# Kernel optimization log

Hardware: AMD Instinct MI355X
Metric: run time of the kernel (lower is better)

Reference implementation:

```python
import jax, jax.numpy as jnp
import numpy as np

EMBED = 1024
HEADS = 16
HEAD_DIM = EMBED // HEADS


def setup_inputs() -> dict:
    key = jax.random.key(0)
    ks = jax.random.split(key, 7)
    N, L = 2, 2048
    values = jax.random.normal(ks[0], (N, L, EMBED), dtype=jnp.float32)
    keys = jax.random.normal(ks[1], (N, L, EMBED), dtype=jnp.float32)
    queries = jax.random.normal(ks[2], (N, L, EMBED), dtype=jnp.float32)
    mask = jax.random.randint(ks[3], (N, 1, L, L), 0, 2, dtype=jnp.int32)
    s = 1.0 / np.sqrt(HEAD_DIM)
    Wv = jax.random.normal(ks[4], (HEAD_DIM, HEAD_DIM), dtype=jnp.float32) * s
    Wk = jax.random.normal(ks[5], (HEAD_DIM, HEAD_DIM), dtype=jnp.float32) * s
    Wq = jax.random.normal(ks[6], (HEAD_DIM, HEAD_DIM), dtype=jnp.float32) * s
    return {"values": values, "keys": keys, "queries": queries, "mask": mask,
            "Wv": Wv, "Wk": Wk, "Wq": Wq}


def reference(values, keys, queries, mask, Wv, Wk, Wq):
    N, Lq = queries.shape[0], queries.shape[1]
    Lk = keys.shape[1]
    # reshape to [N, L, H, D]; nn.Linear(x) = x @ W.T (shared across heads)
    v = values.reshape(N, Lk, HEADS, HEAD_DIM) @ Wv.T
    k = keys.reshape(N, Lk, HEADS, HEAD_DIM) @ Wk.T
    q = queries.reshape(N, Lq, HEADS, HEAD_DIM) @ Wq.T
    # scores scaled by sqrt(embed_size) as in the original module
    e = jnp.einsum("nqhd,nkhd->nhqk", q, k) / jnp.sqrt(jnp.float32(EMBED))
    e = jnp.where(mask == 0, jnp.float32(-1e20), e)
    attn = jax.nn.softmax(e, axis=-1)
    out = jnp.einsum("nhqk,nkhd->nqhd", attn, v)
    return out.reshape(N, Lq, HEADS * HEAD_DIM)
```

## Files before the change

### kernel.cpp

```cpp
#include <hip/hip_runtime.h>
#include <hip/hip_bf16.h>

#define LSEQ 2048
#define NB   2
#define NH   16
#define HD   64
#define NKT  32
#define QSCALE 0.04508687049285173f

typedef __attribute__((ext_vector_type(8))) __bf16 bf16x8;
typedef __attribute__((ext_vector_type(4))) __bf16 bf16x4;
typedef __attribute__((ext_vector_type(2))) __bf16 bf16x2;
typedef __attribute__((ext_vector_type(4))) float  f32x4;

__global__ __launch_bounds__(256)
void pack_mask_kernel(const int* __restrict__ mask,
                      unsigned long long* __restrict__ mbits) {
  size_t gw = ((size_t)blockIdx.x * 256 + threadIdx.x) >> 6;
  int lane = threadIdx.x & 63;
  int v = mask[gw * 64 + lane];
  unsigned long long b = __ballot(v != 0);
  if (lane == 0) mbits[gw] = b;
}

__global__ __launch_bounds__(256)
void proj_kernel(const float* __restrict__ xv, const float* __restrict__ Wv_,
                 const float* __restrict__ xk, const float* __restrict__ Wk_,
                 const float* __restrict__ xq, const float* __restrict__ Wq_,
                 __bf16* __restrict__ outv, __bf16* __restrict__ outk,
                 __bf16* __restrict__ outq) {
  __shared__ __bf16 S[16384];
  __bf16* Xh = S;
  __bf16* Xl = S + 4096;
  __bf16* Wh = S + 8192;
  __bf16* Wl = S + 12288;

  const float* x; const float* W; __bf16* out;
  if (blockIdx.z == 0)      { x = xv; W = Wv_; out = outv; }
  else if (blockIdx.z == 1) { x = xk; W = Wk_; out = outk; }
  else                      { x = xq; W = Wq_; out = outq; }
  const float osc = (blockIdx.z == 2) ? QSCALE : 1.0f;

  const int tid = threadIdx.x;
  const int bx = blockIdx.x;
  const int h  = blockIdx.y;
  const int n  = bx >> 5;
  const int l0 = (bx & 31) << 6;

  const int r  = tid >> 2;
  const int c0 = (tid & 3) << 4;
  const float* xrow = x + ((size_t)(n * LSEQ + l0) + r) * 1024 + h * 64 + c0;
  const float* wrow = W + r * 64 + c0;

#pragma unroll
  for (int hf = 0; hf < 2; ++hf) {
    int kc = c0 + hf * 8;
    int off = r * 64 + (kc ^ ((r & 7) << 3));
    float4 a = *(const float4*)(xrow + hf * 8);
    float4 b = *(const float4*)(xrow + hf * 8 + 4);
    float va[8] = {a.x, a.y, a.z, a.w, b.x, b.y, b.z, b.w};
    bf16x8 hi, lo;
#pragma unroll
    for (int j = 0; j < 8; ++j) {
      __bf16 h_ = (__bf16)va[j];
      hi[j] = h_;
      lo[j] = (__bf16)(va[j] - (float)h_);
    }
    *(bf16x8*)(Xh + off) = hi;
    *(bf16x8*)(Xl + off) = lo;

    float4 c = *(const float4*)(wrow + hf * 8);
    float4 d = *(const float4*)(wrow + hf * 8 + 4);
    float vw[8] = {c.x, c.y, c.z, c.w, d.x, d.y, d.z, d.w};
    bf16x8 whv, wlv;
#pragma unroll
    for (int j = 0; j < 8; ++j) {
      __bf16 h_ = (__bf16)vw[j];
      whv[j] = h_;
      wlv[j] = (__bf16)(vw[j] - (float)h_);
    }
    *(bf16x8*)(Wh + off) = whv;
    *(bf16x8*)(Wl + off) = wlv;
  }
  __syncthreads();

  const int wv   = tid >> 6;
  const int lane = tid & 63;
  const int l15  = lane & 15;
  const int lhi  = lane >> 4;

  bf16x8 xhf[2], xlf[2];
  const int arow = wv * 16 + l15;
#pragma unroll
  for (int ko = 0; ko < 2; ++ko) {
    int aoff = arow * 64 + ((ko * 32 + lhi * 8) ^ ((arow & 7) << 3));
    xhf[ko] = *(const bf16x8*)(Xh + aoff);
    xlf[ko] = *(const bf16x8*)(Xl + aoff);
  }

  f32x4 acc[4] = {};
#pragma unroll
  for (int cg = 0; cg < 4; ++cg) {
    int d = cg * 16 + l15;
#pragma unroll
    for (int ko = 0; ko < 2; ++ko) {
      int boff = d * 64 + ((ko * 32 + lhi * 8) ^ ((d & 7) << 3));
      bf16x8 whf = *(const bf16x8*)(Wh + boff);
      bf16x8 wlf = *(const bf16x8*)(Wl + boff);
      acc[cg] = __builtin_amdgcn_mfma_f32_16x16x32_bf16(xhf[ko], whf, acc[cg], 0, 0, 0);
      acc[cg] = __builtin_amdgcn_mfma_f32_16x16x32_bf16(xhf[ko], wlf, acc[cg], 0, 0, 0);
      acc[cg] = __builtin_amdgcn_mfma_f32_16x16x32_bf16(xlf[ko], whf, acc[cg], 0, 0, 0);
    }
  }
  __syncthreads();

  __bf16* tb = S;
#pragma unroll
  for (int cg = 0; cg < 4; ++cg)
#pragma unroll
    for (int rr = 0; rr < 4; ++rr)
      tb[(wv * 16 + lhi * 4 + rr) * 72 + cg * 16 + l15] = (__bf16)(acc[cg][rr] * osc);
  __syncthreads();

  const int tok = tid >> 2;
  const int d0  = (tid & 3) * 16;
  bf16x8 o0 = *(const bf16x8*)(tb + tok * 72 + d0);
  bf16x8 o1 = *(const bf16x8*)(tb + tok * 72 + d0 + 8);
  size_t ob = (size_t)(n * NH + h) * LSEQ + l0;
  *(bf16x8*)(out + (ob + tok) * HD + d0)     = o0;
  *(bf16x8*)(out + (ob + tok) * HD + d0 + 8) = o1;
}

__global__ __launch_bounds__(256)
void attn_kernel(const __bf16* __restrict__ Qb, const __bf16* __restrict__ Kb,
                 const __bf16* __restrict__ Vb,
                 const unsigned long long* __restrict__ mbits,
                 float* __restrict__ out) {
  __shared__ __bf16 Ks[2][64 * 64];
  __shared__ __bf16 Vts[2][64 * 64];

  const int tid  = threadIdx.x;
  const int wid  = tid >> 6;
  const int lane = tid & 63;
  const int l15  = lane & 15;
  const int lhi  = lane >> 4;

  const int lin = blockIdx.y * 16 + blockIdx.x;
  const int xcd = lin & 7;
  const int idx = lin >> 3;
  const int nh  = xcd + ((idx >> 4) << 3);
  const int qt  = idx & 15;
  const int n   = nh >> 4;
  const int h   = nh & 15;
  const int q0  = qt << 7;

  const __bf16* Qg = Qb + ((size_t)nh * LSEQ + q0) * HD;
  const __bf16* Kg = Kb + (size_t)nh * LSEQ * HD;
  const __bf16* Vg = Vb + (size_t)nh * LSEQ * HD;

  bf16x8 qf[2][2];
#pragma unroll
  for (int mi = 0; mi < 2; ++mi)
#pragma unroll
    for (int ks = 0; ks < 2; ++ks)
      qf[mi][ks] = *(const bf16x8*)(Qg + (size_t)(wid * 32 + mi * 16 + l15) * HD
                                       + ks * 32 + lhi * 8);

  f32x4 o[2][4] = {};
  f32x4 o_ls[2] = {};
  const unsigned long long* mrow0 =
      mbits + ((size_t)n * LSEQ + q0 + wid * 32 + l15) * NKT;
  const unsigned long long* mrow1 = mrow0 + (size_t)16 * NKT;

  bf16x8 onesf;
#pragma unroll
  for (int j = 0; j < 8; ++j) onesf[j] = (__bf16)1.0f;

  const int vkg  = lane & 15;
  const int vdgw = (wid << 2) + lhi;
  const int vslotbase = ((vkg & 8) << 2) + ((vkg & 3) << 3) + (((vkg >> 2) & 1) << 2);
  bf16x4 vv[4];

#define STAGE_K(kt_, buf_)                                                         \
  _Pragma("unroll")                                                                \
  for (int it = 0; it < 2; ++it) {                                                 \
    int chb = wid * 64 + it * 256;                                                 \
    int ch = chb + lane;                                                           \
    int skey = ch >> 3, sdc = ch & 7;                                              \
    const __bf16* src = Kg + (size_t)(kt_) * 4096 + skey * 64 + ((sdc ^ (skey & 7)) << 3); \
    __builtin_amdgcn_global_load_lds(                                              \
        (const __attribute__((address_space(1))) void*)src,                        \
        (__attribute__((address_space(3))) void*)(&Ks[buf_][chb * 8]), 16, 0, 0);  \
  }
#define LOAD_V(kt_)                                                                \
  _Pragma("unroll")                                                                \
  for (int m_ = 0; m_ < 4; ++m_)                                                   \
    vv[m_] = *(const bf16x4*)(Vg + (size_t)(kt_) * 4096 + (vkg * 4 + m_) * HD + vdgw * 4);
#define WRITE_V(buf_)                                                              \
  _Pragma("unroll")                                                                \
  for (int i = 0; i < 4; ++i) {                                                    \
    int d = vdgw * 4 + i;                                                          \
    int swz = (d & 7) ^ ((d >> 3) & 7);                                            \
    bf16x4 pr; pr[0] = vv[0][i]; pr[1] = vv[1][i]; pr[2] = vv[2][i]; pr[3] = vv[3][i]; \
    *(bf16x4*)(&Vts[buf_][d * 64 + (vslotbase ^ (swz << 3))]) = pr;                \
  }

  STAGE_K(0, 0);
  LOAD_V(0);
  WRITE_V(0);
  unsigned long long w0 = mrow0[0];
  unsigned long long w1 = mrow1[0];
  __syncthreads();

  for (int kt = 0; kt < NKT; ++kt) {
    const int cur = kt & 1;
    const int nxt = cur ^ 1;
    const bool pf = (kt + 1 < NKT);
    unsigned long long nw0 = 0, nw1 = 0;
    if (pf) {
      STAGE_K(kt + 1, nxt);
      LOAD_V(kt + 1);
      nw0 = mrow0[kt + 1];
      nw1 = mrow1[kt + 1];
    }

    f32x4 s[2][4] = {};
#pragma unroll
    for (int ks = 0; ks < 2; ++ks)
#pragma unroll
      for (int t = 0; t < 4; ++t) {
        int key = t * 16 + l15;
        bf16x8 kf = *(const bf16x8*)(
            &Ks[cur][key * 64 + ((ks * 32 + lhi * 8) ^ ((key & 7) << 3))]);
        s[0][t] = __builtin_amdgcn_mfma_f32_16x16x32_bf16(kf, qf[0][ks], s[0][t], 0, 0, 0);
        s[1][t] = __builtin_amdgcn_mfma_f32_16x16x32_bf16(kf, qf[1][ks], s[1][t], 0, 0, 0);
      }

    bf16x8 pa[2][2];
#pragma unroll
    for (int mi = 0; mi < 2; ++mi) {
      unsigned long long w = mi ? w1 : w0;
      unsigned long long wsh = w >> (lhi * 4);
      unsigned shl = (unsigned)wsh;
      unsigned shh = (unsigned)(wsh >> 32);
#pragma unroll
      for (int t = 0; t < 4; ++t) {
        unsigned sh = (t < 2) ? shl : shh;
#pragma unroll
        for (int r = 0; r < 4; ++r) {
          float p = __builtin_amdgcn_exp2f(s[mi][t][r]);
          p = ((sh >> ((t & 1) * 16 + r)) & 1u) ? p : 0.f;
          pa[mi][t >> 1][(t & 1) * 4 + r] = (__bf16)p;
        }
      }
    }

    if (pf) { WRITE_V(nxt); }

#pragma unroll
    for (int ks = 0; ks < 2; ++ks) {
#pragma unroll
      for (int t = 0; t < 4; ++t) {
        int d = t * 16 + l15;
        int swz = (d & 7) ^ ((d >> 3) & 7);
        bf16x8 vf = *(const bf16x8*)(
            &Vts[cur][d * 64 + ((ks * 32 + lhi * 8) ^ (swz << 3))]);
        o[0][t] = __builtin_amdgcn_mfma_f32_16x16x32_bf16(pa[0][ks], vf, o[0][t], 0, 0, 0);
        o[1][t] = __builtin_amdgcn_mfma_f32_16x16x32_bf16(pa[1][ks], vf, o[1][t], 0, 0, 0);
      }
      o_ls[0] = __builtin_amdgcn_mfma_f32_16x16x32_bf16(pa[0][ks], onesf, o_ls[0], 0, 0, 0);
      o_ls[1] = __builtin_amdgcn_mfma_f32_16x16x32_bf16(pa[1][ks], onesf, o_ls[1], 0, 0, 0);
    }

    w0 = nw0;
    w1 = nw1;
    __syncthreads();
  }

#pragma unroll
  for (int mi = 0; mi < 2; ++mi) {
    float inv[4];
#pragma unroll
    for (int r = 0; r < 4; ++r)
      inv[r] = 1.f / o_ls[mi][r];
#pragma unroll
    for (int r = 0; r < 4; ++r) {
      size_t ob = ((size_t)n * LSEQ + q0 + wid * 32 + mi * 16 + lhi * 4 + r) * 1024
                + h * 64 + l15;
#pragma unroll
      for (int t = 0; t < 4; ++t)
        out[ob + t * 16] = o[mi][t][r] * inv[r];
    }
  }
#undef STAGE_K
#undef LOAD_V
#undef WRITE_V
}

extern "C" void kernel_launch(void* const* d_in, const int* in_sizes, int n_in,
                              void* d_out, int out_size, void* d_ws, size_t ws_size,
                              hipStream_t stream) {
  const float* xv   = (const float*)d_in[0];
  const float* xk   = (const float*)d_in[1];
  const float* xq   = (const float*)d_in[2];
  const int*   mask = (const int*)d_in[3];
  const float* Wv   = (const float*)d_in[4];
  const float* Wk   = (const float*)d_in[5];
  const float* Wq   = (const float*)d_in[6];
  float* out = (float*)d_out;

  const size_t elems = (size_t)NB * NH * LSEQ * HD;
  __bf16* Qw = (__bf16*)d_ws;
  __bf16* Kw = Qw + elems;
  __bf16* Vw = Kw + elems;
  unsigned long long* mb = (unsigned long long*)(Vw + elems);

  pack_mask_kernel<<<dim3(NB * LSEQ * NKT / 4), 256, 0, stream>>>(mask, mb);
  proj_kernel<<<dim3(64, NH, 3), 256, 0, stream>>>(xv, Wv, xk, Wk, xq, Wq,
                                                   Vw, Kw, Qw);
  attn_kernel<<<dim3(16, 32), 256, 0, stream>>>(Qw, Kw, Vw, mb, out);
}
```

Baseline: 104.5 us.

## Split key tile across two wave groups with LDS reduction of partial outputs

Doubles the attention block to 512 threads. Two groups of four waves each take half of every 64-key tile for the same 128 queries. One group stages K and the other loads and transposes V, which splits the producer work between them. The partial O accumulators and row sums are then combined through LDS at the end. The aim is more waves in flight and shorter per-wave dependency chains, at the cost of an extra reduction pass and higher register and occupancy pressure.

```diff
diff --git a/kernel.cpp b/kernel.cpp
--- a/kernel.cpp
+++ b/kernel.cpp
@@ -131,16 +131,18 @@
   *(bf16x8*)(out + (ob + tok) * HD + d0 + 8) = o1;
 }
 
-__global__ __launch_bounds__(256)
+__global__ __launch_bounds__(512, 4)
 void attn_kernel(const __bf16* __restrict__ Qb, const __bf16* __restrict__ Kb,
                  const __bf16* __restrict__ Vb,
                  const unsigned long long* __restrict__ mbits,
                  float* __restrict__ out) {
-  __shared__ __bf16 Ks[2][64 * 64];
-  __shared__ __bf16 Vts[2][64 * 64];
+  __shared__ __bf16 KV[16384];
+  __shared__ float  Ls[128];
 
   const int tid  = threadIdx.x;
   const int wid  = tid >> 6;
+  const int hw   = wid >> 2;
+  const int wq   = wid & 3;
   const int lane = tid & 63;
   const int l15  = lane & 15;
   const int lhi  = lane >> 4;
@@ -163,13 +165,13 @@
   for (int mi = 0; mi < 2; ++mi)
 #pragma unroll
     for (int ks = 0; ks < 2; ++ks)
-      qf[mi][ks] = *(const bf16x8*)(Qg + (size_t)(wid * 32 + mi * 16 + l15) * HD
+      qf[mi][ks] = *(const bf16x8*)(Qg + (size_t)(wq * 32 + mi * 16 + l15) * HD
                                        + ks * 32 + lhi * 8);
 
   f32x4 o[2][4] = {};
   f32x4 o_ls[2] = {};
   const unsigned long long* mrow0 =
-      mbits + ((size_t)n * LSEQ + q0 + wid * 32 + l15) * NKT;
+      mbits + ((size_t)n * LSEQ + q0 + wq * 32 + l15) * NKT;
   const unsigned long long* mrow1 = mrow0 + (size_t)16 * NKT;
 
   bf16x8 onesf;
@@ -177,20 +179,20 @@
   for (int j = 0; j < 8; ++j) onesf[j] = (__bf16)1.0f;
 
   const int vkg  = lane & 15;
-  const int vdgw = (wid << 2) + lhi;
+  const int vdgw = (wq << 2) + lhi;
   const int vslotbase = ((vkg & 8) << 2) + ((vkg & 3) << 3) + (((vkg >> 2) & 1) << 2);
   bf16x4 vv[4];
 
 #define STAGE_K(kt_, buf_)                                                         \
   _Pragma("unroll")                                                                \
   for (int it = 0; it < 2; ++it) {                                                 \
-    int chb = wid * 64 + it * 256;                                                 \
+    int chb = wq * 64 + it * 256;                                                  \
     int ch = chb + lane;                                                           \
     int skey = ch >> 3, sdc = ch & 7;                                              \
     const __bf16* src = Kg + (size_t)(kt_) * 4096 + skey * 64 + ((sdc ^ (skey & 7)) << 3); \
     __builtin_amdgcn_global_load_lds(                                              \
         (const __attribute__((address_space(1))) void*)src,                        \
-        (__attribute__((address_space(3))) void*)(&Ks[buf_][chb * 8]), 16, 0, 0);  \
+        (__attribute__((address_space(3))) void*)(KV + (buf_) * 4096 + chb * 8), 16, 0, 0); \
   }
 #define LOAD_V(kt_)                                                                \
   _Pragma("unroll")                                                                \
@@ -202,12 +204,11 @@
     int d = vdgw * 4 + i;                                                          \
     int swz = (d & 7) ^ ((d >> 3) & 7);                                            \
     bf16x4 pr; pr[0] = vv[0][i]; pr[1] = vv[1][i]; pr[2] = vv[2][i]; pr[3] = vv[3][i]; \
-    *(bf16x4*)(&Vts[buf_][d * 64 + (vslotbase ^ (swz << 3))]) = pr;                \
-  }
-
-  STAGE_K(0, 0);
-  LOAD_V(0);
-  WRITE_V(0);
+    *(bf16x4*)(KV + 8192 + (buf_) * 4096 + d * 64 + (vslotbase ^ (swz << 3))) = pr; \
+  }
+
+  if (hw == 1) { STAGE_K(0, 0); }
+  else         { LOAD_V(0); WRITE_V(0); }
   unsigned long long w0 = mrow0[0];
   unsigned long long w1 = mrow1[0];
   __syncthreads();
@@ -218,78 +219,90 @@
     const bool pf = (kt + 1 < NKT);
     unsigned long long nw0 = 0, nw1 = 0;
     if (pf) {
-      STAGE_K(kt + 1, nxt);
-      LOAD_V(kt + 1);
+      if (hw == 1) { STAGE_K(kt + 1, nxt); }
+      else         { LOAD_V(kt + 1); }
       nw0 = mrow0[kt + 1];
       nw1 = mrow1[kt + 1];
     }
 
-    f32x4 s[2][4] = {};
+    const __bf16* Kc = KV + cur * 4096;
+    f32x4 s[2][2] = {};
 #pragma unroll
     for (int ks = 0; ks < 2; ++ks)
 #pragma unroll
-      for (int t = 0; t < 4; ++t) {
-        int key = t * 16 + l15;
+      for (int t = 0; t < 2; ++t) {
+        int key = hw * 32 + t * 16 + l15;
         bf16x8 kf = *(const bf16x8*)(
-            &Ks[cur][key * 64 + ((ks * 32 + lhi * 8) ^ ((key & 7) << 3))]);
+            Kc + key * 64 + ((ks * 32 + lhi * 8) ^ ((key & 7) << 3)));
         s[0][t] = __builtin_amdgcn_mfma_f32_16x16x32_bf16(kf, qf[0][ks], s[0][t], 0, 0, 0);
         s[1][t] = __builtin_amdgcn_mfma_f32_16x16x32_bf16(kf, qf[1][ks], s[1][t], 0, 0, 0);
       }
 
-    bf16x8 pa[2][2];
+    bf16x8 pa[2];
 #pragma unroll
     for (int mi = 0; mi < 2; ++mi) {
       unsigned long long w = mi ? w1 : w0;
-      unsigned long long wsh = w >> (lhi * 4);
-      unsigned shl = (unsigned)wsh;
-      unsigned shh = (unsigned)(wsh >> 32);
-#pragma unroll
-      for (int t = 0; t < 4; ++t) {
-        unsigned sh = (t < 2) ? shl : shh;
+      unsigned shl = (unsigned)(w >> (hw * 32 + lhi * 4));
+#pragma unroll
+      for (int t = 0; t < 2; ++t)
 #pragma unroll
         for (int r = 0; r < 4; ++r) {
           float p = __builtin_amdgcn_exp2f(s[mi][t][r]);
-          p = ((sh >> ((t & 1) * 16 + r)) & 1u) ? p : 0.f;
-          pa[mi][t >> 1][(t & 1) * 4 + r] = (__bf16)p;
+          p = ((shl >> (t * 16 + r)) & 1u) ? p : 0.f;
+          pa[mi][t * 4 + r] = (__bf16)p;
         }
-      }
-    }
-
-    if (pf) { WRITE_V(nxt); }
-
-#pragma unroll
-    for (int ks = 0; ks < 2; ++ks) {
-#pragma unroll
-      for (int t = 0; t < 4; ++t) {
-        int d = t * 16 + l15;
-        int swz = (d & 7) ^ ((d >> 3) & 7);
-        bf16x8 vf = *(const bf16x8*)(
-            &Vts[cur][d * 64 + ((ks * 32 + lhi * 8) ^ (swz << 3))]);
-        o[0][t] = __builtin_amdgcn_mfma_f32_16x16x32_bf16(pa[0][ks], vf, o[0][t], 0, 0, 0);
-        o[1][t] = __builtin_amdgcn_mfma_f32_16x16x32_bf16(pa[1][ks], vf, o[1][t], 0, 0, 0);
-      }
-      o_ls[0] = __builtin_amdgcn_mfma_f32_16x16x32_bf16(pa[0][ks], onesf, o_ls[0], 0, 0, 0);
-      o_ls[1] = __builtin_amdgcn_mfma_f32_16x16x32_bf16(pa[1][ks], onesf, o_ls[1], 0, 0, 0);
-    }
+    }
+
+    if (hw == 0 && pf) { WRITE_V(nxt); }
+
+    const __bf16* Vc = KV + 8192 + cur * 4096;
+#pragma unroll
+    for (int t = 0; t < 4; ++t) {
+      int d = t * 16 + l15;
+      int swz = (d & 7) ^ ((d >> 3) & 7);
+      bf16x8 vf = *(const bf16x8*)(
+          Vc + d * 64 + ((hw * 32 + lhi * 8) ^ (swz << 3)));
+      o[0][t] = __builtin_amdgcn_mfma_f32_16x16x32_bf16(pa[0], vf, o[0][t], 0, 0, 0);
+      o[1][t] = __builtin_amdgcn_mfma_f32_16x16x32_bf16(pa[1], vf, o[1][t], 0, 0, 0);
+    }
+    o_ls[0] = __builtin_amdgcn_mfma_f32_16x16x32_bf16(pa[0], onesf, o_ls[0], 0, 0, 0);
+    o_ls[1] = __builtin_amdgcn_mfma_f32_16x16x32_bf16(pa[1], onesf, o_ls[1], 0, 0, 0);
 
     w0 = nw0;
     w1 = nw1;
     __syncthreads();
   }
 
-#pragma unroll
-  for (int mi = 0; mi < 2; ++mi) {
-    float inv[4];
-#pragma unroll
-    for (int r = 0; r < 4; ++r)
-      inv[r] = 1.f / o_ls[mi][r];
-#pragma unroll
-    for (int r = 0; r < 4; ++r) {
-      size_t ob = ((size_t)n * LSEQ + q0 + wid * 32 + mi * 16 + lhi * 4 + r) * 1024
-                + h * 64 + l15;
+  float* Sf = (float*)KV;
+  if (hw == 1) {
+#pragma unroll
+    for (int mi = 0; mi < 2; ++mi) {
 #pragma unroll
       for (int t = 0; t < 4; ++t)
-        out[ob + t * 16] = o[mi][t][r] * inv[r];
+        *(f32x4*)&Sf[wq * 2048 + (mi * 4 + t) * 256 + lane * 4] = o[mi][t];
+      if (l15 == 0)
+        *(f32x4*)&Ls[wq * 32 + mi * 16 + lhi * 4] = o_ls[mi];
+    }
+  }
+  __syncthreads();
+  if (hw == 0) {
+#pragma unroll
+    for (int mi = 0; mi < 2; ++mi) {
+      f32x4 pls = *(const f32x4*)&Ls[wq * 32 + mi * 16 + lhi * 4];
+      float inv[4];
+#pragma unroll
+      for (int r = 0; r < 4; ++r)
+        inv[r] = 1.f / (o_ls[mi][r] + pls[r]);
+#pragma unroll
+      for (int t = 0; t < 4; ++t) {
+        f32x4 po = *(const f32x4*)&Sf[wq * 2048 + (mi * 4 + t) * 256 + lane * 4];
+#pragma unroll
+        for (int r = 0; r < 4; ++r) {
+          size_t ob = ((size_t)n * LSEQ + q0 + wq * 32 + mi * 16 + lhi * 4 + r) * 1024
+                    + h * 64 + t * 16 + l15;
+          out[ob] = (o[mi][t][r] + po[r]) * inv[r];
+        }
+      }
     }
   }
 #undef STAGE_K
@@ -318,5 +331,5 @@
   pack_mask_kernel<<<dim3(NB * LSEQ * NKT / 4), 256, 0, stream>>>(mask, mb);
   proj_kernel<<<dim3(64, NH, 3), 256, 0, stream>>>(xv, Wv, xk, Wk, xq, Wq,
                                                    Vw, Kw, Qw);
-  attn_kernel<<<dim3(16, 32), 256, 0, stream>>>(Qw, Kw, Vw, mb, out);
+  attn_kernel<<<dim3(16, 32), 512, 0, stream>>>(Qw, Kw, Vw, mb, out);
 }
```

Result: no change. 103.1 us (-1.3%).
